# Optimization experiments

Hardware: AMD Instinct MI355X
Metric: run time of the kernel (lower is better)

Reference implementation:

```python
import jax, jax.numpy as jnp
import numpy as np

N = 100000      # n_nodes
D = 64          # in_features == out_features (elementwise W mul requires equality)
DEG = 16        # avg degree for random edges
H = 2           # n_head
ALPHA = 0.2     # LeakyReLU negative slope


def setup_inputs() -> dict:
    key = jax.random.key(0)
    k1, k2, k3 = jax.random.split(key, 3)
    inputs = jax.random.normal(k1, (N, D), dtype=jnp.float32)
    # random edges + self-loops so every row has at least one edge (nonzero rowsum)
    rnd = jax.random.randint(k2, (2, N * DEG), 0, N)
    self_loops = jnp.tile(jnp.arange(N)[None, :], (2, 1))
    edge_index = jnp.concatenate([self_loops, rnd], axis=1)  # [2, 1.7M]
    # per-head params, matching torch init: W = ones, a ~ U(-stdv, stdv)
    W = jnp.ones((H, D), dtype=jnp.float32)
    stdv = 1.0 / np.sqrt(D * 2)
    a = jax.random.uniform(k3, (H, 2 * D), dtype=jnp.float32, minval=-stdv, maxval=stdv)
    return {"inputs": inputs, "edge_index": edge_index, "W": W, "a": a}


def reference(inputs, edge_index, W, a):
    n = inputs.shape[0]
    row, col = edge_index[0], edge_index[1]

    def head(Wh, ah):
        h = inputs * Wh  # [N, D]
        # a @ [h_src; h_dst] decomposes into per-node dots, then scalar edge gather
        score = (h @ ah[:D])[row] + (h @ ah[D:])[col]          # [E]
        e = jnp.exp(jnp.where(score > 0, score, ALPHA * score))  # exp(leaky_relu)
        rowsum = jax.ops.segment_sum(e, row, num_segments=n)     # [N]
        # sparse.mm(coo(edge, e), inputs): h_prime[i] = sum_j e_ij * inputs[j]
        h_prime = jax.ops.segment_sum(e[:, None] * inputs[col], row, num_segments=n)
        return h_prime / rowsum[:, None]

    outs = jax.vmap(head)(W, a)  # [H, N, D]
    return outs.mean(axis=0)
```

## Files before the change

kernel.cpp:

```cpp
#include <hip/hip_runtime.h>


#define D 64
#define ALPHA 0.2f
#define CAP 96
#define BSHIFT 9
#define BROWS 512
#define MAXBUK 256
#define TILE 2048
#define PACKSHIFT 23
#define COLMASK ((1u << PACKSHIFT) - 1u)

__device__ __forceinline__ unsigned bf16rne(float f) {
    unsigned u = __float_as_uint(f);
    u += 0x7fffu + ((u >> 16) & 1u);
    return u >> 16;
}

__global__ __launch_bounds__(256) void k_scores_cast(
    const float* __restrict__ x, const float* __restrict__ W,
    const float* __restrict__ a, float4* __restrict__ s,
    unsigned short* __restrict__ xh, int N)
{
    int wid  = (blockIdx.x * blockDim.x + threadIdx.x) >> 6;
    int lane = threadIdx.x & 63;
    if (wid >= N) return;
    float v = x[(size_t)wid * D + lane];
    xh[(size_t)wid * D + lane] = (unsigned short)bf16rne(v);
    float h0 = v * W[lane];
    float h1 = v * W[D + lane];
    float t0 = h0 * a[lane];
    float t1 = h0 * a[D + lane];
    float t2 = h1 * a[2 * D + lane];
    float t3 = h1 * a[3 * D + lane];
#pragma unroll
    for (int off = 32; off; off >>= 1) {
        t0 += __shfl_xor(t0, off);
        t1 += __shfl_xor(t1, off);
        t2 += __shfl_xor(t2, off);
        t3 += __shfl_xor(t3, off);
    }
    if (lane == 0) s[wid] = make_float4(t0, t1, t2, t3);
}

__global__ __launch_bounds__(256) void k_tile_hist(
    const int* __restrict__ row, unsigned short* __restrict__ tcnt, int E, int nbuk)
{
    __shared__ int h[MAXBUK];
    int t = threadIdx.x, base = blockIdx.x * TILE;
    int cnt = E - base; if (cnt > TILE) cnt = TILE;
    for (int i = t; i < nbuk; i += 256) h[i] = 0;
    __syncthreads();
    for (int i = t; i < cnt; i += 256) atomicAdd(&h[row[base + i] >> BSHIFT], 1);
    __syncthreads();
    for (int i = t; i < nbuk; i += 256)
        tcnt[(size_t)blockIdx.x * MAXBUK + i] = (unsigned short)h[i];
}

__global__ __launch_bounds__(256) void k_col_scan(
    const unsigned short* __restrict__ tcnt, int* __restrict__ tbase,
    int* __restrict__ bcnt, int NT, int nbuk)
{
    __shared__ int wsum[256];
    int b = blockIdx.x, t = threadIdx.x;
    int t4 = t * 4;
    int v0 = (t4     < NT) ? tcnt[(size_t)(t4    ) * MAXBUK + b] : 0;
    int v1 = (t4 + 1 < NT) ? tcnt[(size_t)(t4 + 1) * MAXBUK + b] : 0;
    int v2 = (t4 + 2 < NT) ? tcnt[(size_t)(t4 + 2) * MAXBUK + b] : 0;
    int v3 = (t4 + 3 < NT) ? tcnt[(size_t)(t4 + 3) * MAXBUK + b] : 0;
    int sv = v0 + v1 + v2 + v3;
    wsum[t] = sv;
    __syncthreads();
    for (int off = 1; off < 256; off <<= 1) {
        int add = (t >= off) ? wsum[t - off] : 0;
        __syncthreads();
        wsum[t] += add;
        __syncthreads();
    }
    int run = wsum[t] - sv;
    if (t4     < NT) { tbase[(t4    ) * MAXBUK + b] = run; run += v0; }
    if (t4 + 1 < NT) { tbase[(t4 + 1) * MAXBUK + b] = run; run += v1; }
    if (t4 + 2 < NT) { tbase[(t4 + 2) * MAXBUK + b] = run; run += v2; }
    if (t4 + 3 < NT) { tbase[(t4 + 3) * MAXBUK + b] = run; run += v3; }
    if (t == 255) bcnt[b] = wsum[255];
}

__global__ void k_bucket_scan(const int* __restrict__ bcnt,
                              int* __restrict__ bbase, int nbuk)
{
    __shared__ int sd[MAXBUK];
    int t = threadIdx.x;
    int v = (t < nbuk) ? bcnt[t] : 0;
    sd[t] = v;
    __syncthreads();
    for (int off = 1; off < MAXBUK; off <<= 1) {
        int add = (t >= off) ? sd[t - off] : 0;
        __syncthreads();
        sd[t] += add;
        __syncthreads();
    }
    if (t < nbuk) bbase[t] = sd[t] - v;
    if (t == nbuk - 1) bbase[nbuk] = sd[t];
}

__global__ __launch_bounds__(256) void k_binning(
    const int* __restrict__ row, const int* __restrict__ col,
    const int* __restrict__ bbase, const int* __restrict__ tbase,
    unsigned* __restrict__ ebuf, int E, int nbuk)
{
    __shared__ int lrow[TILE];
    __shared__ int lcol[TILE];
    __shared__ int h[MAXBUK];
    __shared__ int st[MAXBUK];
    __shared__ int gb[MAXBUK];
    __shared__ int cur[MAXBUK];
    __shared__ int sd[MAXBUK];
    int t = threadIdx.x;
    int base = blockIdx.x * TILE;
    int cnt = E - base; if (cnt > TILE) cnt = TILE;

    for (int i = t; i < nbuk; i += 256) h[i] = 0;
    __syncthreads();

    int r[8], c[8], b[8];
#pragma unroll
    for (int j = 0; j < 8; j++) {
        int li = j * 256 + t;
        if (li < cnt) {
            int idx = base + li;
            r[j] = row[idx]; c[j] = col[idx]; b[j] = r[j] >> BSHIFT;
            atomicAdd(&h[b[j]], 1);
        } else b[j] = -1;
    }
    __syncthreads();

    sd[t] = (t < nbuk) ? h[t] : 0;
    __syncthreads();
    for (int off = 1; off < MAXBUK; off <<= 1) {
        int add = (t >= off) ? sd[t - off] : 0;
        __syncthreads();
        sd[t] += add;
        __syncthreads();
    }
    if (t < nbuk) {
        int start = sd[t] - h[t];
        st[t]  = start;
        cur[t] = start;
        gb[t]  = bbase[t] + tbase[blockIdx.x * MAXBUK + t];
    }
    __syncthreads();

#pragma unroll
    for (int j = 0; j < 8; j++) {
        if (b[j] >= 0) {
            int p = atomicAdd(&cur[b[j]], 1);
            lrow[p] = r[j]; lcol[p] = c[j];
        }
    }
    __syncthreads();

    for (int i = t; i < cnt; i += 256) {
        int rr = lrow[i];
        int bb = rr >> BSHIFT;
        ebuf[gb[bb] + (i - st[bb])] =
            ((unsigned)(rr & (BROWS - 1)) << PACKSHIFT) | (unsigned)lcol[i];
    }
}

__global__ __launch_bounds__(1024) void k_rowsort(
    const unsigned* __restrict__ ebuf, const int* __restrict__ bbase,
    int* __restrict__ offsets, int* __restrict__ counts,
    int* __restrict__ scol, int N)
{
    __shared__ int hist[BROWS];
    __shared__ int offs[BROWS];
    __shared__ int wsum[256];
    int b = blockIdx.x, t = threadIdx.x;
    int lo = b << BSHIFT;
    int s0 = bbase[b], s1 = bbase[b + 1];

    if (t < BROWS) hist[t] = 0;
    __syncthreads();
    for (int i = s0 + t; i < s1; i += 1024)
        atomicAdd(&hist[ebuf[i] >> PACKSHIFT], 1);
    __syncthreads();

    int a0 = 0, a1 = 0, sv = 0;
    if (t < 256) { a0 = hist[2 * t]; a1 = hist[2 * t + 1]; sv = a0 + a1; wsum[t] = sv; }
    __syncthreads();
    for (int off = 1; off < 256; off <<= 1) {
        int add = 0;
        if (t < 256 && t >= off) add = wsum[t - off];
        __syncthreads();
        if (t < 256) wsum[t] += add;
        __syncthreads();
    }
    if (t < 256) { int run = wsum[t] - sv; offs[2 * t] = run; offs[2 * t + 1] = run + a0; }
    __syncthreads();

    if (t < BROWS) {
        int rg = lo + t;
        if (rg < N) { offsets[rg] = s0 + offs[t]; counts[rg] = hist[t]; }
    }
    __syncthreads();
    if (t < BROWS) hist[t] = offs[t];
    __syncthreads();

    for (int i = s0 + t; i < s1; i += 1024) {
        unsigned pk = ebuf[i];
        int p = atomicAdd(&hist[pk >> PACKSHIFT], 1);
        scol[s0 + p] = (int)(pk & COLMASK);
    }
}

__global__ __launch_bounds__(256) void k_gather(
    const unsigned* __restrict__ xh2, const float4* __restrict__ s,
    const int* __restrict__ offsets, const int* __restrict__ counts,
    const int* __restrict__ scol, float* __restrict__ out, int N)
{
    __shared__ float  le0[4][CAP];
    __shared__ float  le1[4][CAP];
    __shared__ float2 lpair[4][CAP];
    int w    = threadIdx.x >> 6;
    int lane = threadIdx.x & 63;
    int n    = blockIdx.x * 4 + w;
    bool valid = (n < N);
    int start = 0, cnt = 0;
    float4 srow = make_float4(0.f, 0.f, 0.f, 0.f);
    if (valid) { start = offsets[n]; cnt = counts[n]; srow = s[n]; }

    float sum0 = 0.f, sum1 = 0.f;
    for (int k = lane; k < cnt; k += 64) {
        int c = scol[start + k];
        float4 sc = s[c];
        float sc0 = srow.x + sc.y;
        float sc1 = srow.z + sc.w;
        float e0 = __expf(sc0 > 0.f ? sc0 : ALPHA * sc0);
        float e1 = __expf(sc1 > 0.f ? sc1 : ALPHA * sc1);
        sum0 += e0; sum1 += e1;
        if (k < CAP) { lpair[w][k].x = __int_as_float(c); le0[w][k] = e0; le1[w][k] = e1; }
    }
    int m  = cnt < CAP ? cnt : CAP;
    int mp = (m + 7) & ~7;
    {
        int k = m + lane;
        if (k < mp) { lpair[w][k].x = __int_as_float(0); le0[w][k] = 0.f; le1[w][k] = 0.f; }
    }
#pragma unroll
    for (int off = 32; off; off >>= 1) {
        sum0 += __shfl_xor(sum0, off);
        sum1 += __shfl_xor(sum1, off);
    }
    if (!valid) return;
    float inv0 = 0.5f / sum0, inv1 = 0.5f / sum1;
    for (int k = lane; k < mp; k += 64)
        lpair[w][k].y = inv0 * le0[w][k] + inv1 * le1[w][k];

    int half = lane >> 5;
    int li   = lane & 31;
    float acc0 = 0.f, acc1 = 0.f;
    for (int k = 0; k < mp; k += 8) {
#pragma unroll
        for (int j = 0; j < 4; j++) {
            int kk = k + 2 * j + half;
            float2 pr = lpair[w][kk];
            int c = __float_as_int(pr.x);
            unsigned u = xh2[((unsigned)c << 5) + li];
            acc0 += pr.y * __uint_as_float(u << 16);
            acc1 += pr.y * __uint_as_float(u & 0xffff0000u);
        }
    }
    for (int kk = CAP + half; kk < cnt; kk += 2) {
        int c = scol[start + kk];
        float4 sc = s[c];
        float sc0 = srow.x + sc.y, sc1 = srow.z + sc.w;
        float coef = inv0 * __expf(sc0 > 0.f ? sc0 : ALPHA * sc0)
                   + inv1 * __expf(sc1 > 0.f ? sc1 : ALPHA * sc1);
        unsigned u = xh2[((unsigned)c << 5) + li];
        acc0 += coef * __uint_as_float(u << 16);
        acc1 += coef * __uint_as_float(u & 0xffff0000u);
    }
    acc0 += __shfl_xor(acc0, 32);
    acc1 += __shfl_xor(acc1, 32);
    if (half == 0) {
        float2* o = (float2*)(out + (size_t)n * D);
        o[li] = make_float2(acc0, acc1);
    }
}

extern "C" void kernel_launch(void* const* d_in, const int* in_sizes, int n_in,
                              void* d_out, int out_size, void* d_ws, size_t ws_size,
                              hipStream_t stream)
{
    const float* x  = (const float*)d_in[0];
    const int*   ei = (const int*)d_in[1];
    const float* W  = (const float*)d_in[2];
    const float* a  = (const float*)d_in[3];
    float*       out = (float*)d_out;
    int N = in_sizes[0] / D;
    int E = in_sizes[1] / 2;
    const int* row = ei;
    const int* col = ei + E;

    int NBUK = (N + BROWS - 1) >> BSHIFT;
    int NT   = (E + TILE - 1) / TILE;

    uintptr_t wp = (uintptr_t)d_ws;
    auto alloc = [&wp](size_t bytes) -> void* {
        wp = (wp + 255) & ~(uintptr_t)255;
        void* p = (void*)wp;
        wp += bytes;
        return p;
    };
    unsigned short* xh      = (unsigned short*)alloc((size_t)N * D * 2);
    float4*         s       = (float4*)alloc((size_t)N * sizeof(float4));
    int*            offsets = (int*)alloc((size_t)N * sizeof(int));
    int*            counts  = (int*)alloc((size_t)N * sizeof(int));
    int*            scol    = (int*)alloc((size_t)E * sizeof(int));
    unsigned*       ebuf    = (unsigned*)alloc((size_t)E * sizeof(unsigned));
    int*            tbase   = (int*)alloc((size_t)NT * MAXBUK * sizeof(int));
    int*            bcnt    = (int*)alloc(MAXBUK * sizeof(int));
    int*            bbase   = (int*)alloc((MAXBUK + 4) * sizeof(int));
    unsigned short* tcnt    = (unsigned short*)alloc((size_t)NT * MAXBUK * 2);

    k_scores_cast<<<(N + 3) / 4, 256, 0, stream>>>(x, W, a, s, xh, N);
    k_tile_hist<<<NT, 256, 0, stream>>>(row, tcnt, E, NBUK);
    k_col_scan<<<NBUK, 256, 0, stream>>>(tcnt, tbase, bcnt, NT, NBUK);
    k_bucket_scan<<<1, MAXBUK, 0, stream>>>(bcnt, bbase, NBUK);
    k_binning<<<NT, 256, 0, stream>>>(row, col, bbase, tbase, ebuf, E, NBUK);
    k_rowsort<<<NBUK, 1024, 0, stream>>>(ebuf, bbase, offsets, counts, scol, N);
    k_gather<<<(N + 3) / 4, 256, 0, stream>>>((const unsigned*)xh, s, offsets, counts, scol, out, N);
}
```

Before: 184.3 us.

## Merge score/cast with tile histogram, reuse tile counts in binning, widen gather loads

```diff
diff --git a/kernel.cpp b/kernel.cpp
--- a/kernel.cpp
+++ b/kernel.cpp
@@ -16,50 +16,52 @@
     u += 0x7fffu + ((u >> 16) & 1u);
     return u >> 16;
 }
-
-__global__ __launch_bounds__(256) void k_scores_cast(
+__device__ __forceinline__ float lrexp(float sc) {
+    return __expf(sc > 0.f ? sc : ALPHA * sc);
+}
+
+__global__ __launch_bounds__(256) void k_front(
     const float* __restrict__ x, const float* __restrict__ W,
     const float* __restrict__ a, float4* __restrict__ s,
-    unsigned short* __restrict__ xh, int N)
-{
-    int wid  = (blockIdx.x * blockDim.x + threadIdx.x) >> 6;
-    int lane = threadIdx.x & 63;
-    if (wid >= N) return;
-    float v = x[(size_t)wid * D + lane];
-    xh[(size_t)wid * D + lane] = (unsigned short)bf16rne(v);
-    float h0 = v * W[lane];
-    float h1 = v * W[D + lane];
-    float t0 = h0 * a[lane];
-    float t1 = h0 * a[D + lane];
-    float t2 = h1 * a[2 * D + lane];
-    float t3 = h1 * a[3 * D + lane];
+    unsigned short* __restrict__ xh, const int* __restrict__ row,
+    unsigned short* __restrict__ tcnt, int N, int E, int nblkA)
+{
+    __shared__ int h[MAXBUK];
+    if ((int)blockIdx.x < nblkA) {
+        int wid  = (blockIdx.x * 256 + threadIdx.x) >> 6;
+        int lane = threadIdx.x & 63;
+        if (wid >= N) return;
+        float v = x[(size_t)wid * D + lane];
+        xh[(size_t)wid * D + lane] = (unsigned short)bf16rne(v);
+        float h0 = v * W[lane];
+        float h1 = v * W[D + lane];
+        float t0 = h0 * a[lane];
+        float t1 = h0 * a[D + lane];
+        float t2 = h1 * a[2 * D + lane];
+        float t3 = h1 * a[3 * D + lane];
 #pragma unroll
-    for (int off = 32; off; off >>= 1) {
-        t0 += __shfl_xor(t0, off);
-        t1 += __shfl_xor(t1, off);
-        t2 += __shfl_xor(t2, off);
-        t3 += __shfl_xor(t3, off);
-    }
-    if (lane == 0) s[wid] = make_float4(t0, t1, t2, t3);
-}
-
-__global__ __launch_bounds__(256) void k_tile_hist(
-    const int* __restrict__ row, unsigned short* __restrict__ tcnt, int E, int nbuk)
-{
-    __shared__ int h[MAXBUK];
-    int t = threadIdx.x, base = blockIdx.x * TILE;
-    int cnt = E - base; if (cnt > TILE) cnt = TILE;
-    for (int i = t; i < nbuk; i += 256) h[i] = 0;
-    __syncthreads();
-    for (int i = t; i < cnt; i += 256) atomicAdd(&h[row[base + i] >> BSHIFT], 1);
-    __syncthreads();
-    for (int i = t; i < nbuk; i += 256)
-        tcnt[(size_t)blockIdx.x * MAXBUK + i] = (unsigned short)h[i];
+        for (int off = 32; off; off >>= 1) {
+            t0 += __shfl_xor(t0, off);
+            t1 += __shfl_xor(t1, off);
+            t2 += __shfl_xor(t2, off);
+            t3 += __shfl_xor(t3, off);
+        }
+        if (lane == 0) s[wid] = make_float4(t0, t1, t2, t3);
+    } else {
+        int tile = blockIdx.x - nblkA;
+        int t = threadIdx.x, base = tile * TILE;
+        int cnt = E - base; if (cnt > TILE) cnt = TILE;
+        h[t] = 0;
+        __syncthreads();
+        for (int i = t; i < cnt; i += 256) atomicAdd(&h[row[base + i] >> BSHIFT], 1);
+        __syncthreads();
+        tcnt[(size_t)tile * MAXBUK + t] = (unsigned short)h[t];
+    }
 }
 
 __global__ __launch_bounds__(256) void k_col_scan(
     const unsigned short* __restrict__ tcnt, int* __restrict__ tbase,
-    int* __restrict__ bcnt, int NT, int nbuk)
+    int* __restrict__ bcnt, int NT)
 {
     __shared__ int wsum[256];
     int b = blockIdx.x, t = threadIdx.x;
@@ -78,10 +80,10 @@
         __syncthreads();
     }
     int run = wsum[t] - sv;
-    if (t4     < NT) { tbase[(t4    ) * MAXBUK + b] = run; run += v0; }
-    if (t4 + 1 < NT) { tbase[(t4 + 1) * MAXBUK + b] = run; run += v1; }
-    if (t4 + 2 < NT) { tbase[(t4 + 2) * MAXBUK + b] = run; run += v2; }
-    if (t4 + 3 < NT) { tbase[(t4 + 3) * MAXBUK + b] = run; run += v3; }
+    if (t4     < NT) { tbase[(size_t)(t4    ) * MAXBUK + b] = run; run += v0; }
+    if (t4 + 1 < NT) { tbase[(size_t)(t4 + 1) * MAXBUK + b] = run; run += v1; }
+    if (t4 + 2 < NT) { tbase[(size_t)(t4 + 2) * MAXBUK + b] = run; run += v2; }
+    if (t4 + 3 < NT) { tbase[(size_t)(t4 + 3) * MAXBUK + b] = run; run += v3; }
     if (t == 255) bcnt[b] = wsum[255];
 }
 
@@ -105,57 +107,39 @@
 
 __global__ __launch_bounds__(256) void k_binning(
     const int* __restrict__ row, const int* __restrict__ col,
-    const int* __restrict__ bbase, const int* __restrict__ tbase,
-    unsigned* __restrict__ ebuf, int E, int nbuk)
+    const unsigned short* __restrict__ tcnt, const int* __restrict__ bbase,
+    const int* __restrict__ tbase, unsigned* __restrict__ ebuf, int E)
 {
     __shared__ int lrow[TILE];
     __shared__ int lcol[TILE];
-    __shared__ int h[MAXBUK];
     __shared__ int st[MAXBUK];
     __shared__ int gb[MAXBUK];
     __shared__ int cur[MAXBUK];
-    __shared__ int sd[MAXBUK];
+    __shared__ int wsum[256];
     int t = threadIdx.x;
-    int base = blockIdx.x * TILE;
+    int tile = blockIdx.x;
+    int base = tile * TILE;
     int cnt = E - base; if (cnt > TILE) cnt = TILE;
 
-    for (int i = t; i < nbuk; i += 256) h[i] = 0;
-    __syncthreads();
-
-    int r[8], c[8], b[8];
-#pragma unroll
-    for (int j = 0; j < 8; j++) {
-        int li = j * 256 + t;
-        if (li < cnt) {
-            int idx = base + li;
-            r[j] = row[idx]; c[j] = col[idx]; b[j] = r[j] >> BSHIFT;
-            atomicAdd(&h[b[j]], 1);
-        } else b[j] = -1;
-    }
-    __syncthreads();
-
-    sd[t] = (t < nbuk) ? h[t] : 0;
-    __syncthreads();
-    for (int off = 1; off < MAXBUK; off <<= 1) {
-        int add = (t >= off) ? sd[t - off] : 0;
-        __syncthreads();
-        sd[t] += add;
-        __syncthreads();
-    }
-    if (t < nbuk) {
-        int start = sd[t] - h[t];
-        st[t]  = start;
-        cur[t] = start;
-        gb[t]  = bbase[t] + tbase[blockIdx.x * MAXBUK + t];
-    }
-    __syncthreads();
-
-#pragma unroll
-    for (int j = 0; j < 8; j++) {
-        if (b[j] >= 0) {
-            int p = atomicAdd(&cur[b[j]], 1);
-            lrow[p] = r[j]; lcol[p] = c[j];
-        }
+    int h = tcnt[(size_t)tile * MAXBUK + t];
+    wsum[t] = h;
+    __syncthreads();
+    for (int off = 1; off < 256; off <<= 1) {
+        int add = (t >= off) ? wsum[t - off] : 0;
+        __syncthreads();
+        wsum[t] += add;
+        __syncthreads();
+    }
+    int start = wsum[t] - h;
+    st[t]  = start;
+    cur[t] = start;
+    gb[t]  = bbase[t] + tbase[(size_t)tile * MAXBUK + t];
+    __syncthreads();
+
+    for (int i = t; i < cnt; i += 256) {
+        int r = row[base + i], c = col[base + i];
+        int p = atomicAdd(&cur[r >> BSHIFT], 1);
+        lrow[p] = r; lcol[p] = c;
     }
     __syncthreads();
 
@@ -233,12 +217,10 @@
     for (int k = lane; k < cnt; k += 64) {
         int c = scol[start + k];
         float4 sc = s[c];
-        float sc0 = srow.x + sc.y;
-        float sc1 = srow.z + sc.w;
-        float e0 = __expf(sc0 > 0.f ? sc0 : ALPHA * sc0);
-        float e1 = __expf(sc1 > 0.f ? sc1 : ALPHA * sc1);
+        float e0 = lrexp(srow.x + sc.y);
+        float e1 = lrexp(srow.z + sc.w);
         sum0 += e0; sum1 += e1;
-        if (k < CAP) { lpair[w][k].x = __int_as_float(c); le0[w][k] = e0; le1[w][k] = e1; }
+        if (k < CAP) { lpair[w][k].x = __int_as_float(c << 5); le0[w][k] = e0; le1[w][k] = e1; }
     }
     int m  = cnt < CAP ? cnt : CAP;
     int mp = (m + 7) & ~7;
@@ -256,36 +238,39 @@
     for (int k = lane; k < mp; k += 64)
         lpair[w][k].y = inv0 * le0[w][k] + inv1 * le1[w][k];
 
-    int half = lane >> 5;
-    int li   = lane & 31;
-    float acc0 = 0.f, acc1 = 0.f;
+    int q  = lane >> 4;
+    int li = lane & 15;
+    float a0 = 0.f, a1 = 0.f, a2 = 0.f, a3 = 0.f;
     for (int k = 0; k < mp; k += 8) {
 #pragma unroll
-        for (int j = 0; j < 4; j++) {
-            int kk = k + 2 * j + half;
+        for (int j = 0; j < 2; j++) {
+            int kk = k + 4 * j + q;
             float2 pr = lpair[w][kk];
-            int c = __float_as_int(pr.x);
-            unsigned u = xh2[((unsigned)c << 5) + li];
-            acc0 += pr.y * __uint_as_float(u << 16);
-            acc1 += pr.y * __uint_as_float(u & 0xffff0000u);
+            unsigned cb = (unsigned)__float_as_int(pr.x);
+            uint2 u = *(const uint2*)(xh2 + cb + 2 * li);
+            float cf = pr.y;
+            a0 += cf * __uint_as_float(u.x << 16);
+            a1 += cf * __uint_as_float(u.x & 0xffff0000u);
+            a2 += cf * __uint_as_float(u.y << 16);
+            a3 += cf * __uint_as_float(u.y & 0xffff0000u);
         }
     }
-    for (int kk = CAP + half; kk < cnt; kk += 2) {
+    for (int kk = CAP + q; kk < cnt; kk += 4) {
         int c = scol[start + kk];
         float4 sc = s[c];
-        float sc0 = srow.x + sc.y, sc1 = srow.z + sc.w;
-        float coef = inv0 * __expf(sc0 > 0.f ? sc0 : ALPHA * sc0)
-                   + inv1 * __expf(sc1 > 0.f ? sc1 : ALPHA * sc1);
-        unsigned u = xh2[((unsigned)c << 5) + li];
-        acc0 += coef * __uint_as_float(u << 16);
-        acc1 += coef * __uint_as_float(u & 0xffff0000u);
-    }
-    acc0 += __shfl_xor(acc0, 32);
-    acc1 += __shfl_xor(acc1, 32);
-    if (half == 0) {
-        float2* o = (float2*)(out + (size_t)n * D);
-        o[li] = make_float2(acc0, acc1);
-    }
+        float cf = inv0 * lrexp(srow.x + sc.y) + inv1 * lrexp(srow.z + sc.w);
+        uint2 u = *(const uint2*)(xh2 + ((unsigned)c << 5) + 2 * li);
+        a0 += cf * __uint_as_float(u.x << 16);
+        a1 += cf * __uint_as_float(u.x & 0xffff0000u);
+        a2 += cf * __uint_as_float(u.y << 16);
+        a3 += cf * __uint_as_float(u.y & 0xffff0000u);
+    }
+    a0 += __shfl_xor(a0, 16); a0 += __shfl_xor(a0, 32);
+    a1 += __shfl_xor(a1, 16); a1 += __shfl_xor(a1, 32);
+    a2 += __shfl_xor(a2, 16); a2 += __shfl_xor(a2, 32);
+    a3 += __shfl_xor(a3, 16); a3 += __shfl_xor(a3, 32);
+    if (q == 0)
+        ((float4*)(out + (size_t)n * D))[li] = make_float4(a0, a1, a2, a3);
 }
 
 extern "C" void kernel_launch(void* const* d_in, const int* in_sizes, int n_in,
@@ -323,11 +308,11 @@
     int*            bbase   = (int*)alloc((MAXBUK + 4) * sizeof(int));
     unsigned short* tcnt    = (unsigned short*)alloc((size_t)NT * MAXBUK * 2);
 
-    k_scores_cast<<<(N + 3) / 4, 256, 0, stream>>>(x, W, a, s, xh, N);
-    k_tile_hist<<<NT, 256, 0, stream>>>(row, tcnt, E, NBUK);
-    k_col_scan<<<NBUK, 256, 0, stream>>>(tcnt, tbase, bcnt, NT, NBUK);
+    int nblkA = (N + 3) / 4;
+    k_front<<<nblkA + NT, 256, 0, stream>>>(x, W, a, s, xh, row, tcnt, N, E, nblkA);
+    k_col_scan<<<NBUK, 256, 0, stream>>>(tcnt, tbase, bcnt, NT);
     k_bucket_scan<<<1, MAXBUK, 0, stream>>>(bcnt, bbase, NBUK);
-    k_binning<<<NT, 256, 0, stream>>>(row, col, bbase, tbase, ebuf, E, NBUK);
+    k_binning<<<NT, 256, 0, stream>>>(row, col, tcnt, bbase, tbase, ebuf, E);
     k_rowsort<<<NBUK, 1024, 0, stream>>>(ebuf, bbase, offsets, counts, scol, N);
     k_gather<<<(N + 3) / 4, 256, 0, stream>>>((const unsigned*)xh, s, offsets, counts, scol, out, N);
 }
```

Measured after the change: 188.3 us. 1.02x slower.
